# Kernel tuning notes

Hardware: AMD Instinct MI355X
Metric: run time of the kernel (lower is better)

## Reference

```python
import jax, jax.numpy as jnp
import numpy as np


def _wn_dense_relu(x, v, g, bias):
    # torch weight_norm over dim=0: w[h,:] = g[h] * v[h,:] / ||v[h,:]||
    w = g[:, None] * v / jnp.linalg.norm(v, axis=1, keepdims=True)  # (hid, inp)
    return jax.nn.relu(jnp.einsum('bld,hd->blh', x, w) + bias)


def _masked_softmax(scores, mask, axis):
    # additive large-negative masking, numerically stable softmax
    return jax.nn.softmax(scores + jnp.where(mask > 0, 0.0, -1e9), axis=axis)


def setup_inputs() -> dict:
    key = jax.random.key(0)
    ks = jax.random.split(key, 6)
    B, La, Lb, D, H = 8, 2048, 2048, 256, 256
    return {
        'a': jax.random.normal(ks[0], (B, La, D), dtype=jnp.float32),
        'b': jax.random.normal(ks[1], (B, Lb, D), dtype=jnp.float32),
        'mask_a': jax.random.randint(ks[2], (B, La), 0, 2, dtype=jnp.int32),
        'mask_b': jax.random.randint(ks[3], (B, Lb), 0, 2, dtype=jnp.int32),
        'a_v': jax.random.normal(ks[4], (H, D), dtype=jnp.float32) * (2.0 / D) ** 0.5,
        'a_g': jnp.ones((H,), dtype=jnp.float32),
        'a_bias': jnp.zeros((H,), dtype=jnp.float32),
        'b_v': jax.random.normal(ks[5], (H, D), dtype=jnp.float32) * (2.0 / D) ** 0.5,
        'b_g': jnp.ones((H,), dtype=jnp.float32),
        'b_bias': jnp.zeros((H,), dtype=jnp.float32),
        'tau': jnp.asarray((1.0 / H) ** 0.5, dtype=jnp.float32),
    }


def reference(a, b, mask_a, mask_b, a_v, a_g, a_bias, b_v, b_g, b_bias, tau):
    ha = _wn_dense_relu(a, a_v, a_g, a_bias)                 # (B, La, H)
    hb = _wn_dense_relu(b, b_v, b_g, b_bias)                 # (B, Lb, H)
    attn = jnp.einsum('bih,bjh->bij', ha, hb) * tau          # (B, La, Lb)
    weight_a = _masked_softmax(attn, mask_a[:, :, None], axis=1)  # softmax over La
    weight_b = _masked_softmax(attn, mask_b[:, None, :], axis=2)  # softmax over Lb
    align_a = jnp.einsum('bij,bjd->bid', weight_b, b)        # (B, La, D)
    align_b = jnp.einsum('bij,bid->bjd', weight_a, a)        # (B, Lb, D)
    return align_a, align_b
```

## Files before the change

### kernel.cpp

```cpp
#include <hip/hip_runtime.h>
#include <hip/hip_bf16.h>
#include <stdint.h>

#define B_   8
#define L_   2048
#define D_   256
#define H_   256
#define TJ   64
#define NT   (L_/TJ)
#define BM   64
#define LOG2E 1.4426950408889634f

typedef short bf16x8 __attribute__((ext_vector_type(8)));
typedef short bf16x4 __attribute__((ext_vector_type(4)));
typedef unsigned short u16x4 __attribute__((ext_vector_type(4)));
typedef float f32x4  __attribute__((ext_vector_type(4)));

#define MFMA(a,b,c) __builtin_amdgcn_mfma_f32_16x16x32_bf16(a,b,c,0,0,0)
#define EX2(x) __builtin_amdgcn_exp2f(x)

typedef unsigned int u32;
__device__ __forceinline__ void gload_lds16(const void* g, void* l){
  __builtin_amdgcn_global_load_lds((const __attribute__((address_space(1))) u32*)g,
                                   (__attribute__((address_space(3))) u32*)l, 16, 0, 0);
}

__device__ __forceinline__ unsigned short f2bf(float f){
  __hip_bfloat16 h = __float2bfloat16(f);
  unsigned short us;
  __builtin_memcpy(&us, &h, 2);
  return us;
}
__device__ __forceinline__ float bf2f(unsigned short u){
  u32 t = ((u32)u) << 16;
  float f;
  __builtin_memcpy(&f, &t, 4);
  return f;
}

__device__ __forceinline__ void bar_lgkm(){
  asm volatile("s_waitcnt lgkmcnt(0)" ::: "memory");
  __builtin_amdgcn_s_barrier();
  __builtin_amdgcn_sched_barrier(0);
}
__device__ __forceinline__ void bar_all(){
  asm volatile("s_waitcnt vmcnt(0) lgkmcnt(0)" ::: "memory");
  __builtin_amdgcn_s_barrier();
  __builtin_amdgcn_sched_barrier(0);
}

__global__ __launch_bounds__(256) void wnorm_kernel(const float* __restrict__ av,
      const float* __restrict__ ag, const float* __restrict__ bv,
      const float* __restrict__ bg, unsigned short* __restrict__ wa,
      unsigned short* __restrict__ wb, float* __restrict__ maxn){
  int sel = blockIdx.y;
  if (blockIdx.x == 0 && threadIdx.x < 8) maxn[sel*8 + threadIdx.x] = 0.f;
  const float* v = sel ? bv : av;
  const float* g = sel ? bg : ag;
  unsigned short* w = sel ? wb : wa;
  int h = blockIdx.x;
  int d = threadIdx.x;
  float x = v[h*D_ + d];
  float sq = x*x;
  for (int off = 32; off; off >>= 1) sq += __shfl_down(sq, off, 64);
  __shared__ float red[4];
  int lane = threadIdx.x & 63, wid = threadIdx.x >> 6;
  if (lane == 0) red[wid] = sq;
  __syncthreads();
  float tot = red[0] + red[1] + red[2] + red[3];
  float scale = g[h] / sqrtf(tot);
  w[h*D_ + d] = f2bf(x * scale);
}

__global__ __launch_bounds__(256) void hgemm_kernel(const float* __restrict__ a,
      const float* __restrict__ b, const unsigned short* __restrict__ wa,
      const unsigned short* __restrict__ wb, const float* __restrict__ a_bias,
      const float* __restrict__ b_bias, const float* __restrict__ tau_ptr,
      unsigned short* __restrict__ ha, unsigned short* __restrict__ hb,
      unsigned short* __restrict__ aT, unsigned short* __restrict__ bT,
      float* __restrict__ rn_a, float* __restrict__ rn_b,
      float* __restrict__ maxn){
  __shared__ __align__(16) unsigned short xlk[64][256];
  __shared__ float redp[2][2][32];
  __shared__ float redm[4];
  int sel = blockIdx.y;
  const float* x = sel ? b : a;
  const unsigned short* w = sel ? wb : wa;
  const float* bias = sel ? b_bias : a_bias;
  unsigned short* hx = sel ? hb : ha;
  unsigned short* xT = sel ? bT : aT;
  float* rn = sel ? rn_b : rn_a;
  float scale = sel ? 1.0f : tau_ptr[0] * LOG2E;
  int m0 = blockIdx.x * 64;
  int bz = m0 / L_, l0 = m0 % L_;
  int tid = threadIdx.x;
  int lane = tid & 63, wid = tid >> 6;
  int rp = wid >> 1, ch = wid & 1;
  int p = lane & 15, q = lane >> 4;

  {
    int r0 = tid >> 6;
    int c  = (tid & 63) * 4;
    int slot = c >> 3, half = (c >> 2) & 1;
    #pragma unroll
    for (int it = 0; it < 16; ++it){
      int row = it*4 + r0;
      f32x4 v = *(const f32x4*)(x + (size_t)(m0 + row) * 256 + c);
      uint2 wv;
      wv.x = (u32)f2bf(v[0]) | ((u32)f2bf(v[1]) << 16);
      wv.y = (u32)f2bf(v[2]) | ((u32)f2bf(v[3]) << 16);
      *(uint2*)((char*)&xlk[row][0] + ((slot ^ (row & 7)) << 4) + half*8) = wv;
    }
  }
  __syncthreads();

  bf16x8 af[2][8];
  #pragma unroll
  for (int g = 0; g < 2; ++g){
    int row = rp*32 + g*16 + p;
    #pragma unroll
    for (int kk = 0; kk < 8; ++kk)
      af[g][kk] = *(const bf16x8*)((char*)&xlk[row][0] + (((kk*4 + q) ^ (row & 7)) << 4));
  }
  f32x4 acc[2][8];
  #pragma unroll
  for (int g = 0; g < 2; ++g)
    #pragma unroll
    for (int n = 0; n < 8; ++n) acc[g][n] = (f32x4){0.f,0.f,0.f,0.f};
  #pragma unroll
  for (int kk = 0; kk < 8; kk++){
    #pragma unroll
    for (int n = 0; n < 8; n++){
      bf16x8 bfr = *(const bf16x8*)(w + (size_t)(ch*128 + n*16 + p) * 256 + kk*32 + q*8);
      acc[0][n] = MFMA(af[0][kk], bfr, acc[0][n]);
      acc[1][n] = MFMA(af[1][kk], bfr, acc[1][n]);
    }
  }

  #pragma unroll
  for (int it = 0; it < 16; it++){
    int d = it*16 + (tid >> 4);
    int c = (tid & 15) * 4;
    bf16x4 v;
    #pragma unroll
    for (int j = 0; j < 4; j++){
      int row = c + j;
      v[j] = (short)*((const unsigned short*)((char*)&xlk[row][0]
                + (((d >> 3) ^ (row & 7)) << 4)) + (d & 7));
    }
    *(bf16x4*)(xT + ((size_t)bz*D_ + d)*L_ + l0 + c) = v;
  }
  __syncthreads();

  unsigned short* hl = &xlk[0][0];
  float rs[2][4] = {{0.f,0.f,0.f,0.f},{0.f,0.f,0.f,0.f}};
  #pragma unroll
  for (int g = 0; g < 2; ++g)
    #pragma unroll
    for (int n = 0; n < 8; ++n){
      float bv = bias[ch*128 + n*16 + p];
      #pragma unroll
      for (int r = 0; r < 4; ++r){
        int row = rp*32 + g*16 + q*4 + r;
        float vv = acc[g][n][r] + bv;
        vv = vv > 0.f ? vv : 0.f;
        float sv = vv * scale;
        rs[g][r] += sv * sv;
        hl[row*256 + ch*128 + n*16 + p] = f2bf(sv);
      }
    }
  #pragma unroll
  for (int off = 1; off < 16; off <<= 1)
    #pragma unroll
    for (int g = 0; g < 2; ++g)
      #pragma unroll
      for (int r = 0; r < 4; r++)
        rs[g][r] += __shfl_xor(rs[g][r], off, 64);
  if (p == 0){
    #pragma unroll
    for (int g = 0; g < 2; ++g)
      #pragma unroll
      for (int r = 0; r < 4; ++r)
        redp[ch][rp][g*16 + q*4 + r] = rs[g][r];
  }
  __syncthreads();

  float lmax = 0.f;
  #pragma unroll
  for (int g = 0; g < 2; ++g)
    #pragma unroll
    for (int r = 0; r < 4; ++r){
      int idx = g*16 + q*4 + r;
      float tot = redp[0][rp][idx] + redp[1][rp][idx];
      float rv = sqrtf(tot) * 1.01f;
      lmax = fmaxf(lmax, rv);
      if (ch == 0 && p == 0) rn[m0 + rp*32 + idx] = rv;
    }
  lmax = fmaxf(lmax, __shfl_xor(lmax, 16, 64));
  lmax = fmaxf(lmax, __shfl_xor(lmax, 32, 64));
  if (lane == 0) redm[wid] = lmax;

  #pragma unroll
  for (int i = 0; i < 8; ++i){
    int idx = i*256 + tid;
    bf16x8 hv = *(const bf16x8*)(hl + idx*8);
    *(bf16x8*)(hx + (size_t)m0*256 + (size_t)idx*8) = hv;
  }
  __syncthreads();
  if (tid == 0){
    float bm = fmaxf(fmaxf(redm[0], redm[1]), fmaxf(redm[2], redm[3]));
    atomicMax((u32*)&maxn[sel*8 + bz], __float_as_uint(bm));
  }
}

__global__ __launch_bounds__(256, 2) void flash_kernel(
    const unsigned short* __restrict__ ha, const unsigned short* __restrict__ hb,
    const unsigned short* __restrict__ aT, const unsigned short* __restrict__ bT,
    const int* __restrict__ mask_a, const int* __restrict__ mask_b,
    const float* __restrict__ rn_a, const float* __restrict__ rn_b,
    const float* __restrict__ maxn, float* __restrict__ out)
{
  __shared__ __align__(16) unsigned short HBT[64][256];
  __shared__ __align__(16) unsigned short VTL[256][64];
  __shared__ __align__(16) unsigned short WT[2][32][64];
  __shared__ unsigned short MSKB[2048];
  __shared__ float SST[4][32];

  const int bid = blockIdx.x;
  const int s   = bid & 15;
  const int dir = s >> 3;
  const int bz  = s & 7;
  const int i0  = (bid >> 4) * BM;
  const int tid = threadIdx.x;
  const int lane = tid & 63;
  const int wid  = tid >> 6;
  const int wr = wid >> 1, wc = wid & 1;
  const int p = lane & 15, q = lane >> 4;

  const unsigned short* hA = dir ? hb : ha;
  const unsigned short* hB = dir ? ha : hb;
  const unsigned short* vT = dir ? aT : bT;
  const int* mask = dir ? mask_a : mask_b;
  const float* rnA = dir ? rn_b : rn_a;
  const float mxB  = maxn[(dir ^ 1)*8 + bz];
  float* outp = out + ((size_t)dir * B_ + bz) * L_ * D_;

  const unsigned short* hAp = hA + (size_t)bz * L_ * H_;
  const unsigned short* hBp = hB + (size_t)bz * L_ * H_;
  const unsigned short* vTp = vT + (size_t)bz * D_ * L_;
  const int* mp = mask + bz * L_;

  const int hb_r0 = tid >> 5;
  const int hb_s  = tid & 31;
  const int vt_r0 = tid >> 3;
  const int vt_s  = tid & 7;

  bf16x8 af[2][8];
  #pragma unroll
  for (int g = 0; g < 2; ++g)
    #pragma unroll
    for (int kk = 0; kk < 8; ++kk)
      af[g][kk] = *(const bf16x8*)(hAp + (size_t)(i0 + wr*32 + g*16 + p) * H_ + kk*32 + q*8);

  float m_p[2];
  #pragma unroll
  for (int g = 0; g < 2; ++g)
    m_p[g] = rnA[bz*L_ + i0 + wr*32 + g*16 + p] * mxB;

  #pragma unroll
  for (int i = 0; i < 8; ++i){
    int idx = tid + i*256;
    MSKB[idx] = f2bf((mp[idx] > 0) ? 0.f : -1e9f);
  }

  f32x4 acc[2][8];
  #pragma unroll
  for (int g = 0; g < 2; ++g)
    #pragma unroll
    for (int n = 0; n < 8; ++n) acc[g][n] = (f32x4){0.f,0.f,0.f,0.f};
  float s_run[2];
  s_run[0] = s_run[1] = 0.f;

  #define STAGE_HB(jj0) do {                                                      \
    _Pragma("unroll")                                                             \
    for (int k = 0; k < 8; ++k){                                                  \
      int rr = k*8 + hb_r0;                                                       \
      int sp = hb_s ^ (rr & 7);                                                   \
      gload_lds16(hBp + (size_t)((jj0) + rr) * H_ + sp*8,                         \
                  &HBT[0][0] + k*2048 + tid*8);                                   \
    }                                                                             \
  } while(0)
  #define STAGE_VT(jj0) do {                                                      \
    _Pragma("unroll")                                                             \
    for (int k = 0; k < 8; ++k){                                                  \
      int rr = k*32 + vt_r0;                                                      \
      int sp = vt_s ^ (rr & 7);                                                   \
      gload_lds16(vTp + (size_t)rr * L_ + (jj0) + sp*8,                           \
                  &VTL[0][0] + k*2048 + tid*8);                                   \
    }                                                                             \
  } while(0)

  STAGE_HB(0);
  STAGE_VT(0);
  bar_all();

  for (int jt = 0; jt < NT; ++jt){
    const int j0 = jt * TJ;

    f32x4 accp[2][2];
    #pragma unroll
    for (int g = 0; g < 2; ++g)
      #pragma unroll
      for (int cg = 0; cg < 2; ++cg) accp[g][cg] = (f32x4){0.f,0.f,0.f,0.f};
    __builtin_amdgcn_s_setprio(1);
    #pragma unroll
    for (int kk = 0; kk < 8; ++kk){
      const int rb = wc*32 + p;
      const int sp = ((kk*4 + q) ^ (p & 7)) * 8;
      bf16x8 b0 = *(const bf16x8*)(&HBT[0][0] + rb*256 + sp);
      bf16x8 b1 = *(const bf16x8*)(&HBT[0][0] + (rb+16)*256 + sp);
      accp[0][0] = MFMA(b0, af[0][kk], accp[0][0]);
      accp[1][0] = MFMA(b0, af[1][kk], accp[1][0]);
      accp[0][1] = MFMA(b1, af[0][kk], accp[0][1]);
      accp[1][1] = MFMA(b1, af[1][kk], accp[1][1]);
    }
    __builtin_amdgcn_s_setprio(0);

    u16x4 k0 = *(const u16x4*)(&MSKB[j0 + wc*32 + q*4]);
    u16x4 k1 = *(const u16x4*)(&MSKB[j0 + wc*32 + 16 + q*4]);
    f32x4 mm0, mm1;
    #pragma unroll
    for (int r = 0; r < 4; ++r){ mm0[r] = bf2f(k0[r]); mm1[r] = bf2f(k1[r]); }

    #pragma unroll
    for (int g = 0; g < 2; ++g){
      #pragma unroll
      for (int cg = 0; cg < 2; ++cg){
        const f32x4 mm = cg ? mm1 : mm0;
        float w0 = EX2(accp[g][cg][0] + mm[0] - m_p[g]);
        float w1 = EX2(accp[g][cg][1] + mm[1] - m_p[g]);
        float w2 = EX2(accp[g][cg][2] + mm[2] - m_p[g]);
        float w3 = EX2(accp[g][cg][3] + mm[3] - m_p[g]);
        s_run[g] += (w0 + w1) + (w2 + w3);
        uint2 wv;
        wv.x = (u32)f2bf(w0) | ((u32)f2bf(w1) << 16);
        wv.y = (u32)f2bf(w2) | ((u32)f2bf(w3) << 16);
        int row = g*16 + p;
        int sl  = (wc*4 + cg*2 + (q>>1)) ^ (row & 7);
        *(uint2*)(&WT[wr][0][0] + row*64 + (sl<<3) + ((q&1)<<2)) = wv;
      }
    }
    bar_lgkm();

    if (jt + 1 < NT) STAGE_HB(j0 + TJ);

    bf16x8 wf[2][2];
    #pragma unroll
    for (int g = 0; g < 2; ++g)
      #pragma unroll
      for (int ks = 0; ks < 2; ++ks){
        int row = g*16 + p;
        wf[g][ks] = *(const bf16x8*)(&WT[wr][0][0] + row*64
                                     + ((((ks*4 + q) ^ (row & 7)))<<3));
      }

    __builtin_amdgcn_s_setprio(1);
    #pragma unroll
    for (int n = 0; n < 8; ++n){
      const int d = wc*128 + n*16 + p;
      #pragma unroll
      for (int ks = 0; ks < 2; ++ks){
        const int sp = ((ks*4 + q) ^ (d & 7)) * 8;
        bf16x8 vf = *(const bf16x8*)(&VTL[0][0] + d*64 + sp);
        acc[0][n] = MFMA(wf[0][ks], vf, acc[0][n]);
        acc[1][n] = MFMA(wf[1][ks], vf, acc[1][n]);
      }
    }
    __builtin_amdgcn_s_setprio(0);

    bar_all();
    if (jt + 1 < NT){
      STAGE_VT(j0 + TJ);
      bar_all();
    }
  }
  #undef STAGE_HB
  #undef STAGE_VT

  s_run[0] += __shfl_xor(s_run[0], 16, 64);
  s_run[0] += __shfl_xor(s_run[0], 32, 64);
  s_run[1] += __shfl_xor(s_run[1], 16, 64);
  s_run[1] += __shfl_xor(s_run[1], 32, 64);
  if (q == 0){
    SST[wid][p]      = s_run[0];
    SST[wid][16 + p] = s_run[1];
  }
  __syncthreads();
  float invS[2][4];
  #pragma unroll
  for (int g = 0; g < 2; ++g)
    #pragma unroll
    for (int r = 0; r < 4; ++r){
      int idx = g*16 + q*4 + r;
      invS[g][r] = 1.0f / (SST[wr*2][idx] + SST[wr*2 + 1][idx]);
    }

  #pragma unroll
  for (int g = 0; g < 2; ++g)
    #pragma unroll
    for (int n = 0; n < 8; ++n)
      #pragma unroll
      for (int r = 0; r < 4; ++r){
        int row = i0 + wr*32 + g*16 + q*4 + r;
        outp[(size_t)row * D_ + wc*128 + n*16 + p] = acc[g][n][r] * invS[g][r];
      }
}

extern "C" void kernel_launch(void* const* d_in, const int* in_sizes, int n_in,
                              void* d_out, int out_size, void* d_ws, size_t ws_size,
                              hipStream_t stream) {
  const float* a      = (const float*)d_in[0];
  const float* b      = (const float*)d_in[1];
  const int*   mask_a = (const int*)d_in[2];
  const int*   mask_b = (const int*)d_in[3];
  const float* a_v    = (const float*)d_in[4];
  const float* a_g    = (const float*)d_in[5];
  const float* a_bias = (const float*)d_in[6];
  const float* b_v    = (const float*)d_in[7];
  const float* b_g    = (const float*)d_in[8];
  const float* b_bias = (const float*)d_in[9];
  const float* tau    = (const float*)d_in[10];

  float* out = (float*)d_out;

  char* ws = (char*)d_ws;
  const size_t SZ_W  = (size_t)H_ * D_ * 2;
  const size_t SZ_H  = (size_t)B_ * L_ * H_ * 2;
  unsigned short* wa = (unsigned short*)(ws);
  unsigned short* wb = (unsigned short*)(ws + SZ_W);
  unsigned short* ha = (unsigned short*)(ws + 2*SZ_W);
  unsigned short* hb = (unsigned short*)(ws + 2*SZ_W + SZ_H);
  unsigned short* aT = (unsigned short*)(ws + 2*SZ_W + 2*SZ_H);
  unsigned short* bT = (unsigned short*)(ws + 2*SZ_W + 3*SZ_H);
  float* rn_a = (float*)(ws + 2*SZ_W + 4*SZ_H);
  float* rn_b = rn_a + (size_t)B_ * L_;
  float* maxn = rn_b + (size_t)B_ * L_;
  size_t need = 2*SZ_W + 4*SZ_H + 2*(size_t)B_*L_*4 + 64;
  if (ws_size < need) return;

  wnorm_kernel<<<dim3(H_, 2), 256, 0, stream>>>(a_v, a_g, b_v, b_g, wa, wb, maxn);

  {
    dim3 g((B_*L_)/64, 2);
    hgemm_kernel<<<g, 256, 0, stream>>>(a, b, wa, wb, a_bias, b_bias, tau,
                                        ha, hb, aT, bT, rn_a, rn_b, maxn);
  }

  {
    flash_kernel<<<dim3((L_/BM) * B_ * 2), 256, 0, stream>>>(
        ha, hb, aT, bT, mask_a, mask_b, rn_a, rn_b, maxn, out);
  }
}
```

Measured before the change: 121.8 us.

## Software-pipeline flash loop with double-buffered LDS and halved key tile

Restructures the flash attention loop into a software pipeline. The QK^T scores and exponentials for tile t+1 are computed while the PV MFMAs for tile t run, and HB/V tiles are double-buffered in LDS so there is one barrier per iteration instead of two to three. The key tile shrinks from 64 to 32, and the mask is stored as ballot bitmasks rather than a bf16 array. This doubles the iteration count and adds register pressure, in exchange for hiding global-load and exp latency behind MFMA work.

```diff
diff --git a/kernel.cpp b/kernel.cpp
--- a/kernel.cpp
+++ b/kernel.cpp
@@ -6,14 +6,13 @@
 #define L_   2048
 #define D_   256
 #define H_   256
-#define TJ   64
+#define TJ   32
 #define NT   (L_/TJ)
 #define BM   64
 #define LOG2E 1.4426950408889634f
 
 typedef short bf16x8 __attribute__((ext_vector_type(8)));
 typedef short bf16x4 __attribute__((ext_vector_type(4)));
-typedef unsigned short u16x4 __attribute__((ext_vector_type(4)));
 typedef float f32x4  __attribute__((ext_vector_type(4)));
 
 #define MFMA(a,b,c) __builtin_amdgcn_mfma_f32_16x16x32_bf16(a,b,c,0,0,0)
@@ -31,18 +30,7 @@
   __builtin_memcpy(&us, &h, 2);
   return us;
 }
-__device__ __forceinline__ float bf2f(unsigned short u){
-  u32 t = ((u32)u) << 16;
-  float f;
-  __builtin_memcpy(&f, &t, 4);
-  return f;
-}
-
-__device__ __forceinline__ void bar_lgkm(){
-  asm volatile("s_waitcnt lgkmcnt(0)" ::: "memory");
-  __builtin_amdgcn_s_barrier();
-  __builtin_amdgcn_sched_barrier(0);
-}
+
 __device__ __forceinline__ void bar_all(){
   asm volatile("s_waitcnt vmcnt(0) lgkmcnt(0)" ::: "memory");
   __builtin_amdgcn_s_barrier();
@@ -220,10 +208,10 @@
     const float* __restrict__ rn_a, const float* __restrict__ rn_b,
     const float* __restrict__ maxn, float* __restrict__ out)
 {
-  __shared__ __align__(16) unsigned short HBT[64][256];
-  __shared__ __align__(16) unsigned short VTL[256][64];
-  __shared__ __align__(16) unsigned short WT[2][32][64];
-  __shared__ unsigned short MSKB[2048];
+  __shared__ __align__(16) unsigned short HBT[2][8192];
+  __shared__ __align__(16) unsigned short VP [2][8192];
+  __shared__ __align__(16) unsigned short WT [2][2560];
+  __shared__ u32 MSKW[64];
   __shared__ float SST[4][32];
 
   const int bid = blockIdx.x;
@@ -250,11 +238,6 @@
   const unsigned short* vTp = vT + (size_t)bz * D_ * L_;
   const int* mp = mask + bz * L_;
 
-  const int hb_r0 = tid >> 5;
-  const int hb_s  = tid & 31;
-  const int vt_r0 = tid >> 3;
-  const int vt_s  = tid & 7;
-
   bf16x8 af[2][8];
   #pragma unroll
   for (int g = 0; g < 2; ++g)
@@ -268,9 +251,10 @@
     m_p[g] = rnA[bz*L_ + i0 + wr*32 + g*16 + p] * mxB;
 
   #pragma unroll
-  for (int i = 0; i < 8; ++i){
-    int idx = tid + i*256;
-    MSKB[idx] = f2bf((mp[idx] > 0) ? 0.f : -1e9f);
+  for (int k = 0; k < 8; ++k){
+    int idx = wid*8 + k;
+    unsigned long long bb = __ballot(mp[idx*64 + lane] > 0);
+    if (lane == 0){ MSKW[idx*2] = (u32)bb; MSKW[idx*2+1] = (u32)(bb >> 32); }
   }
 
   f32x4 acc[2][8];
@@ -281,111 +265,103 @@
   float s_run[2];
   s_run[0] = s_run[1] = 0.f;
 
-  #define STAGE_HB(jj0) do {                                                      \
+  #define STAGE_HB(bb, jj0) do {                                                  \
     _Pragma("unroll")                                                             \
-    for (int k = 0; k < 8; ++k){                                                  \
-      int rr = k*8 + hb_r0;                                                       \
-      int sp = hb_s ^ (rr & 7);                                                   \
+    for (int k = 0; k < 4; ++k){                                                  \
+      int rr = k*8 + (tid >> 5);                                                  \
+      int sp = (tid & 31) ^ (rr & 7);                                             \
       gload_lds16(hBp + (size_t)((jj0) + rr) * H_ + sp*8,                         \
-                  &HBT[0][0] + k*2048 + tid*8);                                   \
+                  &HBT[bb][0] + k*2048 + tid*8);                                  \
     }                                                                             \
   } while(0)
-  #define STAGE_VT(jj0) do {                                                      \
+  #define STAGE_VP(bb, jj0) do {                                                  \
     _Pragma("unroll")                                                             \
-    for (int k = 0; k < 8; ++k){                                                  \
-      int rr = k*32 + vt_r0;                                                      \
-      int sp = vt_s ^ (rr & 7);                                                   \
-      gload_lds16(vTp + (size_t)rr * L_ + (jj0) + sp*8,                           \
-                  &VTL[0][0] + k*2048 + tid*8);                                   \
+    for (int k = 0; k < 4; ++k){                                                  \
+      int c = k*256 + tid;                                                        \
+      int R = c >> 3, ph = c & 7;                                                 \
+      int l = ph ^ (R & 7);                                                       \
+      int d = 2*R + (l >> 2);                                                     \
+      int jj = (l & 3) * 8;                                                       \
+      gload_lds16(vTp + (size_t)d * L_ + (jj0) + jj,                              \
+                  &VP[bb][0] + c*8);                                              \
     }                                                                             \
   } while(0)
 
-  STAGE_HB(0);
-  STAGE_VT(0);
+  #define QK_TILE(buf, accp) do {                                                 \
+    _Pragma("unroll")                                                             \
+    for (int kk = 0; kk < 8; ++kk){                                               \
+      const int rb = wc*16 + p;                                                   \
+      const int sp = ((kk*4 + q) ^ (p & 7)) * 8;                                  \
+      bf16x8 b0 = *(const bf16x8*)(&HBT[buf][0] + rb*256 + sp);                   \
+      accp[0] = MFMA(b0, af[0][0+kk], accp[0]);                                   \
+      accp[1] = MFMA(b0, af[1][0+kk], accp[1]);                                   \
+    }                                                                             \
+  } while(0)
+
+  #define EXP_WT(tt, wb, accp) do {                                               \
+    u32 mw = MSKW[tt];                                                            \
+    _Pragma("unroll")                                                             \
+    for (int g = 0; g < 2; ++g){                                                  \
+      float ww[4];                                                                \
+      _Pragma("unroll")                                                           \
+      for (int r = 0; r < 4; ++r){                                                \
+        float mm = ((mw >> (wc*16 + q*4 + r)) & 1u) ? 0.f : -1e9f;                \
+        ww[r] = EX2(accp[g][r] + mm - m_p[g]);                                    \
+      }                                                                           \
+      s_run[g] += (ww[0] + ww[1]) + (ww[2] + ww[3]);                              \
+      uint2 wv;                                                                   \
+      wv.x = (u32)f2bf(ww[0]) | ((u32)f2bf(ww[1]) << 16);                         \
+      wv.y = (u32)f2bf(ww[2]) | ((u32)f2bf(ww[3]) << 16);                         \
+      int row = g*16 + p;                                                         \
+      *(uint2*)((char*)&WT[wb][0] + (wr*1280 + row*40 + wc*16 + q*4)*2) = wv;     \
+    }                                                                             \
+  } while(0)
+
+  STAGE_HB(0, 0);
+  STAGE_VP(0, 0);
+  STAGE_HB(1, TJ);
   bar_all();
-
-  for (int jt = 0; jt < NT; ++jt){
-    const int j0 = jt * TJ;
-
-    f32x4 accp[2][2];
-    #pragma unroll
-    for (int g = 0; g < 2; ++g)
-      #pragma unroll
-      for (int cg = 0; cg < 2; ++cg) accp[g][cg] = (f32x4){0.f,0.f,0.f,0.f};
+  {
+    f32x4 accp[2] = {(f32x4){0.f,0.f,0.f,0.f}, (f32x4){0.f,0.f,0.f,0.f}};
     __builtin_amdgcn_s_setprio(1);
-    #pragma unroll
-    for (int kk = 0; kk < 8; ++kk){
-      const int rb = wc*32 + p;
-      const int sp = ((kk*4 + q) ^ (p & 7)) * 8;
-      bf16x8 b0 = *(const bf16x8*)(&HBT[0][0] + rb*256 + sp);
-      bf16x8 b1 = *(const bf16x8*)(&HBT[0][0] + (rb+16)*256 + sp);
-      accp[0][0] = MFMA(b0, af[0][kk], accp[0][0]);
-      accp[1][0] = MFMA(b0, af[1][kk], accp[1][0]);
-      accp[0][1] = MFMA(b1, af[0][kk], accp[0][1]);
-      accp[1][1] = MFMA(b1, af[1][kk], accp[1][1]);
-    }
+    QK_TILE(0, accp);
     __builtin_amdgcn_s_setprio(0);
-
-    u16x4 k0 = *(const u16x4*)(&MSKB[j0 + wc*32 + q*4]);
-    u16x4 k1 = *(const u16x4*)(&MSKB[j0 + wc*32 + 16 + q*4]);
-    f32x4 mm0, mm1;
-    #pragma unroll
-    for (int r = 0; r < 4; ++r){ mm0[r] = bf2f(k0[r]); mm1[r] = bf2f(k1[r]); }
-
+    EXP_WT(0, 0, accp);
+  }
+
+  for (int t = 0; t < NT; ++t){
+    bar_all();
+    const int cb = t & 1;
+
+    bf16x8 wf[2];
     #pragma unroll
     for (int g = 0; g < 2; ++g){
-      #pragma unroll
-      for (int cg = 0; cg < 2; ++cg){
-        const f32x4 mm = cg ? mm1 : mm0;
-        float w0 = EX2(accp[g][cg][0] + mm[0] - m_p[g]);
-        float w1 = EX2(accp[g][cg][1] + mm[1] - m_p[g]);
-        float w2 = EX2(accp[g][cg][2] + mm[2] - m_p[g]);
-        float w3 = EX2(accp[g][cg][3] + mm[3] - m_p[g]);
-        s_run[g] += (w0 + w1) + (w2 + w3);
-        uint2 wv;
-        wv.x = (u32)f2bf(w0) | ((u32)f2bf(w1) << 16);
-        wv.y = (u32)f2bf(w2) | ((u32)f2bf(w3) << 16);
-        int row = g*16 + p;
-        int sl  = (wc*4 + cg*2 + (q>>1)) ^ (row & 7);
-        *(uint2*)(&WT[wr][0][0] + row*64 + (sl<<3) + ((q&1)<<2)) = wv;
-      }
-    }
-    bar_lgkm();
-
-    if (jt + 1 < NT) STAGE_HB(j0 + TJ);
-
-    bf16x8 wf[2][2];
-    #pragma unroll
-    for (int g = 0; g < 2; ++g)
-      #pragma unroll
-      for (int ks = 0; ks < 2; ++ks){
-        int row = g*16 + p;
-        wf[g][ks] = *(const bf16x8*)(&WT[wr][0][0] + row*64
-                                     + ((((ks*4 + q) ^ (row & 7)))<<3));
-      }
-
+      int row = g*16 + p;
+      wf[g] = *(const bf16x8*)((char*)&WT[cb][0] + (wr*1280 + row*40 + q*8)*2);
+    }
+
+    if (t + 2 < NT) STAGE_HB(cb, (t+2)*TJ);
+    if (t + 1 < NT) STAGE_VP(cb ^ 1, (t+1)*TJ);
+
+    f32x4 accp[2] = {(f32x4){0.f,0.f,0.f,0.f}, (f32x4){0.f,0.f,0.f,0.f}};
     __builtin_amdgcn_s_setprio(1);
+    if (t + 1 < NT) QK_TILE(cb ^ 1, accp);
     #pragma unroll
     for (int n = 0; n < 8; ++n){
       const int d = wc*128 + n*16 + p;
-      #pragma unroll
-      for (int ks = 0; ks < 2; ++ks){
-        const int sp = ((ks*4 + q) ^ (d & 7)) * 8;
-        bf16x8 vf = *(const bf16x8*)(&VTL[0][0] + d*64 + sp);
-        acc[0][n] = MFMA(wf[0][ks], vf, acc[0][n]);
-        acc[1][n] = MFMA(wf[1][ks], vf, acc[1][n]);
-      }
+      const int R = d >> 1;
+      const int ph = ((d & 1)*4 + q) ^ (R & 7);
+      bf16x8 vf = *(const bf16x8*)(&VP[cb][0] + R*64 + ph*8);
+      acc[0][n] = MFMA(wf[0], vf, acc[0][n]);
+      acc[1][n] = MFMA(wf[1], vf, acc[1][n]);
     }
     __builtin_amdgcn_s_setprio(0);
-
-    bar_all();
-    if (jt + 1 < NT){
-      STAGE_VT(j0 + TJ);
-      bar_all();
-    }
+    if (t + 1 < NT) EXP_WT(t+1, cb ^ 1, accp);
   }
   #undef STAGE_HB
-  #undef STAGE_VT
+  #undef STAGE_VP
+  #undef QK_TILE
+  #undef EXP_WT
 
   s_run[0] += __shfl_xor(s_run[0], 16, 64);
   s_run[0] += __shfl_xor(s_run[0], 32, 64);
```

Result: slower. 131.4 us (+7.9%).
